# Kernel optimization log

Measured on AMD Instinct MI355X. Metric: run time of the kernel, lower is better.

## Reference

```python
import jax, jax.numpy as jnp
import numpy as np

N_HEADS = 4
D_HEAD = 16
SCALE = D_HEAD ** 0.5  # NOTE: original multiplies by sqrt(d_head), faithful


def _mha(x, Wq, bq, Wk, bk, Wv, bv, Wo, bo):
    # x: (..., N, D) with D = N_HEADS * D_HEAD
    q = jnp.einsum('...nd,od->...no', x, Wq) + bq
    k = jnp.einsum('...nd,od->...no', x, Wk) + bk
    v = jnp.einsum('...nd,od->...no', x, Wv) + bv
    lead = x.shape[:-2]
    n = x.shape[-2]
    q = q.reshape(*lead, n, N_HEADS, D_HEAD)
    k = k.reshape(*lead, n, N_HEADS, D_HEAD)
    v = v.reshape(*lead, n, N_HEADS, D_HEAD)
    scores = jnp.einsum('...nhd,...mhd->...hnm', q, k) * SCALE
    attn = jax.nn.softmax(scores, axis=-1)
    o = jnp.einsum('...hnm,...mhd->...nhd', attn, v).reshape(*lead, n, N_HEADS * D_HEAD)
    return jnp.einsum('...nd,od->...no', o, Wo) + bo


def setup_inputs() -> dict:
    key = jax.random.key(0)
    ks = jax.random.split(key, 20)
    b, n, d, dhf, G, C = 16, 16384, 64, 64, 256, 64
    s = 0.05
    inp = {
        'x': jax.random.normal(ks[0], (b, n, d), dtype=jnp.float32),
        'partitions': jax.random.permutation(ks[1], n).reshape(G, C).astype(jnp.int64),
    }
    names = ['q_intra', 'k_intra', 'v_intra', 'o_intra',
             'q_inter', 'k_inter', 'v_inter', 'o_inter']
    for i, nm in enumerate(names):
        d_in = d if nm.endswith('intra') and nm[0] != 'o' else dhf
        inp['W' + nm] = jax.random.normal(ks[2 + 2 * i], (dhf, d_in), dtype=jnp.float32) * s
        inp['b' + nm] = jax.random.normal(ks[3 + 2 * i], (dhf,), dtype=jnp.float32) * s
    return inp


def reference(x, partitions,
              Wq_intra, bq_intra, Wk_intra, bk_intra, Wv_intra, bv_intra, Wo_intra, bo_intra,
              Wq_inter, bq_inter, Wk_inter, bk_inter, Wv_inter, bv_inter, Wo_inter, bo_inter):
    b = x.shape[0]
    G, C = partitions.shape
    dhf = Wq_intra.shape[0]
    # gather nodes into groups: (b, G, C, d)
    xg = x[:, partitions, :]
    # intra-group attention, vectorized over (b, G)
    intra = _mha(xg, Wq_intra, bq_intra, Wk_intra, bk_intra,
                 Wv_intra, bv_intra, Wo_intra, bo_intra)  # (b, G, C, dhf)
    # MaxPool1d(kernel=dhf) over token axis with C == dhf -> max over tokens
    pooled = jnp.max(intra, axis=2)  # (b, G, dhf)
    inter = _mha(pooled, Wq_inter, bq_inter, Wk_inter, bk_inter,
                 Wv_inter, bv_inter, Wo_inter, bo_inter)  # (b, G, dhf)
    # broadcast-add inter-group features to every token in the group
    out = intra + inter[:, :, None, :]  # (b, G, C, dhf)
    flat = out.reshape(b, G * C, dhf)
    inv = jnp.argsort(partitions.reshape(-1))  # restore original node order
    return flat[:, inv, :]
```

## Files before the change

### kernel.cpp

```cpp
#include <hip/hip_runtime.h>
#include <hip/hip_bf16.h>

#define NTOK 16384
#define NG   256
#define NB   16

typedef float  f32x4   __attribute__((ext_vector_type(4)));
typedef short  short8v __attribute__((ext_vector_type(8)));
typedef short  short4v __attribute__((ext_vector_type(4)));

#define MFMA_BF16(a, b, c) __builtin_amdgcn_mfma_f32_16x16x32_bf16((a), (b), (c), 0, 0, 0)

#define QSCALE 5.770780163555856f

__device__ __forceinline__ short f2bf(float f) {
    union { float f; unsigned u; } x; x.f = f;
    unsigned r = (x.u + 0x7FFF + ((x.u >> 16) & 1)) >> 16;
    return (short)r;
}
__device__ __forceinline__ short bft(float f) {
    union { float f; unsigned u; } x; x.f = f;
    return (short)(x.u >> 16);
}
__device__ __forceinline__ float bf2f(short s) {
    union { float f; unsigned u; } x;
    x.u = ((unsigned)(unsigned short)s) << 16;
    return x.f;
}
__device__ __forceinline__ float u2f(unsigned u) {
    union { unsigned u; float f; } x; x.u = u; return x.f;
}
__device__ __forceinline__ unsigned pk_cvt(float a, float b) {
#if __has_builtin(__builtin_amdgcn_cvt_pk_bf16_f32)
    auto r = __builtin_amdgcn_cvt_pk_bf16_f32(a, b);
    unsigned u; __builtin_memcpy(&u, &r, 4); return u;
#else
    union { float f; unsigned u; } xa, xb; xa.f = a; xb.f = b;
    const unsigned ua = xa.u + (0x7FFFu + ((xa.u >> 16) & 1));
    const unsigned ub = xb.u + (0x7FFFu + ((xb.u >> 16) & 1));
    return __builtin_amdgcn_perm(ub, ua, 0x07060302u);
#endif
}

__global__ void k_setup(const int* __restrict__ raw, int* __restrict__ part,
                        const float* __restrict__ Wq, const float* __restrict__ Wk,
                        const float* __restrict__ Wv, const float* __restrict__ Wo,
                        const float* __restrict__ Wqe, const float* __restrict__ Wke,
                        const float* __restrict__ Wve, const float* __restrict__ Woe,
                        short8v* __restrict__ wf)
{
    const int gid = blockIdx.x * 256 + threadIdx.x;
    if (gid < 16384) {
        const bool is64 = (raw[1] == 0 && raw[3] == 0 && raw[5] == 0);
        part[gid] = is64 ? raw[2 * gid] : raw[gid];
        return;
    }
    const int p = gid - 16384;
    if (p >= 5632) return;
    if (p < 3584) {
        const int v    = p >> 9;
        const int rem  = p & 511;
        const int tau  = rem >> 6;
        const int lane = rem & 63;
        const int jt = tau >> 1, kt = tau & 1;
        const int o  = jt * 16 + (lane & 15);
        const int d0 = kt * 32 + (lane >> 4) * 8;
        const float* W = (v < 2) ? Wq : (v < 4) ? Wk : (v < 6) ? Wv : Wo;
        const bool lo = (v & 1) && (v < 6);
        short8v r8;
#pragma unroll
        for (int i = 0; i < 8; ++i) {
            const float f = W[o * 64 + d0 + i];
            const short hh = f2bf(f);
            r8[i] = lo ? f2bf(f - bf2f(hh)) : hh;
        }
        wf[p] = r8;
    } else {
        const int g2   = p - 3584;
        const int v    = g2 >> 9;
        const int rem  = g2 & 511;
        const int tau  = rem >> 6;
        const int lane = rem & 63;
        const int jt = tau >> 1, kt = tau & 1;
        const int o  = jt * 16 + (lane & 15);
        const int d0 = kt * 32 + (lane >> 4) * 8;
        const float* W = (v == 0) ? Wqe : (v == 1) ? Wke : (v == 2) ? Wve : Woe;
        short8v r8;
#pragma unroll
        for (int i = 0; i < 8; ++i) r8[i] = f2bf(W[o * 64 + d0 + i]);
        wf[p] = r8;
    }
}

__global__ __launch_bounds__(256, 4) void k_intra(
    const float* __restrict__ x, const int* __restrict__ part,
    const short8v* __restrict__ wf,
    const float* __restrict__ bq, const float* __restrict__ bk,
    const float* __restrict__ bv, const float* __restrict__ bo,
    float* __restrict__ out, float* __restrict__ pooled,
    unsigned short* __restrict__ intra_g, const int use_g)
{
    __shared__ __align__(16) short S[20480];

    short* const xh = S;
    short* const kk = S + 4096;
    short* const ql = S + 8192;
    short* const qh = S + 12288;
    short* const vT = S + 16384;

    const int t  = threadIdx.x;
    const int g  = blockIdx.x;
    const int bb = blockIdx.y;
    const int l  = t & 63;
    const int w  = t >> 6;
    const int quad = l >> 4;
    const int col  = l & 15;

    for (int j = t; j < 512; j += 256) {
        const int row = j >> 3, c8 = j & 7;
        const int tok = part[g * 64 + row];
        const float* px = x + ((size_t)bb * NTOK + tok) * 64 + c8 * 8;
        const float4 f0 = ((const float4*)px)[0];
        const float4 f1 = ((const float4*)px)[1];
        uint4 pk;
        pk.x = pk_cvt(f0.x, f0.y);
        pk.y = pk_cvt(f0.z, f0.w);
        pk.z = pk_cvt(f1.x, f1.y);
        pk.w = pk_cvt(f1.z, f1.w);
        *(uint4*)&xh[row * 64 + ((c8 ^ (row & 7)) << 3)] = pk;
    }
    __syncthreads();

    {
        const f32x4 bq4 = *(const f32x4*)&bq[w * 16 + quad * 4];
        const f32x4 bk4 = *(const f32x4*)&bk[w * 16 + quad * 4];
        const float bvv = bv[w * 16 + col];
        f32x4 bqs;
#pragma unroll
        for (int r = 0; r < 4; ++r) bqs[r] = bq4[r] * QSCALE;
        short8v bqh[2], bql2[2], bkh[2], bkl[2], bvh[2], bvl[2];
#pragma unroll
        for (int kt = 0; kt < 2; ++kt) {
            const int tau = w * 2 + kt;
            bqh[kt]  = wf[(0 * 8 + tau) * 64 + l];
            bql2[kt] = wf[(1 * 8 + tau) * 64 + l];
            bkh[kt]  = wf[(2 * 8 + tau) * 64 + l];
            bkl[kt]  = wf[(3 * 8 + tau) * 64 + l];
            bvh[kt]  = wf[(4 * 8 + tau) * 64 + l];
            bvl[kt]  = wf[(5 * 8 + tau) * 64 + l];
        }
        for (int mt = 0; mt < 4; ++mt) {
            short8v axh[2];
#pragma unroll
            for (int kt = 0; kt < 2; ++kt) {
                const int row = mt * 16 + col;
                axh[kt] = *(const short8v*)&xh[row * 64 + (((kt * 4 + quad) ^ (row & 7)) << 3)];
            }
            f32x4 aq = {0.f, 0.f, 0.f, 0.f};
            f32x4 ak = {0.f, 0.f, 0.f, 0.f};
            f32x4 av = {0.f, 0.f, 0.f, 0.f};
#pragma unroll
            for (int kt = 0; kt < 2; ++kt) {
                aq = MFMA_BF16(bqh[kt],  axh[kt], aq);
                aq = MFMA_BF16(bql2[kt], axh[kt], aq);
                ak = MFMA_BF16(bkh[kt],  axh[kt], ak);
                ak = MFMA_BF16(bkl[kt],  axh[kt], ak);
                av = MFMA_BF16(axh[kt], bvh[kt],  av);
                av = MFMA_BF16(axh[kt], bvl[kt],  av);
            }
            f32x4 q4;
#pragma unroll
            for (int r = 0; r < 4; ++r) q4[r] = fmaf(aq[r], QSCALE, bqs[r]);
            const unsigned qh01 = pk_cvt(q4[0], q4[1]);
            const unsigned qh23 = pk_cvt(q4[2], q4[3]);
            const float lo0 = q4[0] - u2f(qh01 << 16);
            const float lo1 = q4[1] - u2f(qh01 & 0xFFFF0000u);
            const float lo2 = q4[2] - u2f(qh23 << 16);
            const float lo3 = q4[3] - u2f(qh23 & 0xFFFF0000u);
            const unsigned ql01 = pk_cvt(lo0, lo1);
            const unsigned ql23 = pk_cvt(lo2, lo3);
            const unsigned k01 = pk_cvt(ak[0] + bk4[0], ak[1] + bk4[1]);
            const unsigned k23 = pk_cvt(ak[2] + bk4[2], ak[3] + bk4[3]);
            const int m = mt * 16 + col;
            const int pos = m * 64 + (((w * 2 + (quad >> 1)) ^ (m & 7)) << 3) + ((quad & 1) << 2);
            uint2 uq; uq.x = qh01; uq.y = qh23;
            uint2 ulo; ulo.x = ql01; ulo.y = ql23;
            uint2 uk; uk.x = k01; uk.y = k23;
            *(uint2*)&qh[pos] = uq;
            *(uint2*)&ql[pos] = ulo;
            *(uint2*)&kk[pos] = uk;
            {
                const int d = w * 16 + col;
                uint2 v4;
                v4.x = pk_cvt(av[0] + bvv, av[1] + bvv);
                v4.y = pk_cvt(av[2] + bvv, av[3] + bvv);
                const int cm = mt * 2 + (quad >> 1);
                const int idx = d * 64 + ((cm ^ (d & 7)) << 3) + ((quad & 1) * 4);
                *(uint2*)&vT[idx] = v4;
            }
        }
    }

    const int h = w, hc = h * 16;
    f32x4 s[4][4];
    {
        short8v ak4[4];
#pragma unroll
        for (int it = 0; it < 4; ++it) {
            const int row = it * 16 + col;
            ak4[it] = *(const short8v*)&kk[row * 64 + (((h * 2 + (quad & 1)) ^ (row & 7)) << 3)];
        }
        const short8v z8 = {0, 0, 0, 0, 0, 0, 0, 0};
        for (int jt = 0; jt < 4; ++jt) {
            const int row = jt * 16 + col;
            const int idx = row * 64 + (((h * 2 + (quad & 1)) ^ (row & 7)) << 3);
            short8v bqh_ = *(const short8v*)&qh[idx];
            short8v bql_ = *(const short8v*)&ql[idx];
            if (quad >= 2) { bqh_ = z8; bql_ = z8; }
#pragma unroll
            for (int it = 0; it < 4; ++it) {
                f32x4 acc = {0.f, 0.f, 0.f, 0.f};
                acc = MFMA_BF16(ak4[it], bqh_, acc);
                acc = MFMA_BF16(ak4[it], bql_, acc);
                s[it][jt] = acc;
            }
        }
    }
    float rden[4];
#pragma unroll
    for (int jt = 0; jt < 4; ++jt) {
        float ds = 0.f;
#pragma unroll
        for (int it = 0; it < 4; ++it) {
#pragma unroll
            for (int r = 0; r < 4; ++r) {
                const float e = exp2f(s[it][jt][r]);
                s[it][jt][r] = e;
                ds += e;
            }
        }
        ds += __shfl_xor(ds, 16);
        ds += __shfl_xor(ds, 32);
        rden[jt] = 1.0f / ds;
    }
    __syncthreads();

    f32x4 oa[4];
#pragma unroll
    for (int jt = 0; jt < 4; ++jt) oa[jt] = (f32x4){0.f, 0.f, 0.f, 0.f};
    short* const Pw = S + w * 2560;
    for (int kt = 0; kt < 2; ++kt) {
#pragma unroll
        for (int jt = 0; jt < 4; ++jt) {
#pragma unroll
            for (int ih = 0; ih < 2; ++ih) {
                const int it = kt * 2 + ih;
                uint2 pp;
                pp.x = pk_cvt(s[it][jt][0], s[it][jt][1]);
                pp.y = pk_cvt(s[it][jt][2], s[it][jt][3]);
                *(uint2*)&Pw[(jt * 16 + col) * 40 + ih * 16 + (quad << 2)] = pp;
            }
        }
        const int dv = hc + col;
        const int cmv = kt * 4 + quad;
        const short8v av8 = *(const short8v*)&vT[dv * 64 + ((cmv ^ (dv & 7)) << 3)];
#pragma unroll
        for (int jt = 0; jt < 4; ++jt) {
            const short8v bp = *(const short8v*)&Pw[(jt * 16 + col) * 40 + (quad << 3)];
            oa[jt] = MFMA_BF16(av8, bp, oa[jt]);
        }
    }
#pragma unroll
    for (int jt = 0; jt < 4; ++jt) {
        const float rd = rden[jt];
        const unsigned o01 = pk_cvt(oa[jt][0] * rd, oa[jt][1] * rd);
        const unsigned o23 = pk_cvt(oa[jt][2] * rd, oa[jt][3] * rd);
        const int m = jt * 16 + col;
        const int pos = m * 64 + (((w * 2 + (quad >> 1)) ^ (m & 7)) << 3) + ((quad & 1) << 2);
        uint2 ov; ov.x = o01; ov.y = o23;
        *(uint2*)&qh[pos] = ov;
    }
    __syncthreads();

    float* const os = (float*)S;
    {
        const float bov = bo[w * 16 + col];
        short8v bo8[2];
        bo8[0] = wf[(6 * 8 + w * 2 + 0) * 64 + l];
        bo8[1] = wf[(6 * 8 + w * 2 + 1) * 64 + l];
        float pm = -1e30f;
        for (int mt = 0; mt < 4; ++mt) {
            f32x4 acc = {0.f, 0.f, 0.f, 0.f};
#pragma unroll
            for (int kt = 0; kt < 2; ++kt) {
                const int row = mt * 16 + col;
                const short8v ao = *(const short8v*)&qh[row * 64 + (((kt * 4 + quad) ^ (row & 7)) << 3)];
                acc = MFMA_BF16(ao, bo8[kt], acc);
            }
#pragma unroll
            for (int r = 0; r < 4; ++r) {
                const float vo = acc[r] + bov;
                pm = fmaxf(pm, vo);
                os[(mt * 16 + quad * 4 + r) * 68 + w * 16 + col] = vo;
            }
        }
        pm = fmaxf(pm, __shfl_xor(pm, 16));
        pm = fmaxf(pm, __shfl_xor(pm, 32));
        if (l < 16)
            pooled[((size_t)bb * NG + g) * 64 + w * 16 + col] = pm;
    }
    __syncthreads();

    {
        const int row = t >> 2, seg = t & 3;
        const float* pr = &os[row * 68 + seg * 16];
        const f32x4 v0 = ((const f32x4*)pr)[0];
        const f32x4 v1 = ((const f32x4*)pr)[1];
        const f32x4 v2 = ((const f32x4*)pr)[2];
        const f32x4 v3 = ((const f32x4*)pr)[3];
        if (use_g) {
            uint4 p0, p1;
            p0.x = pk_cvt(v0[0], v0[1]); p0.y = pk_cvt(v0[2], v0[3]);
            p0.z = pk_cvt(v1[0], v1[1]); p0.w = pk_cvt(v1[2], v1[3]);
            p1.x = pk_cvt(v2[0], v2[1]); p1.y = pk_cvt(v2[2], v2[3]);
            p1.z = pk_cvt(v3[0], v3[1]); p1.w = pk_cvt(v3[2], v3[3]);
            unsigned short* dst = &intra_g[(((size_t)bb * NG + g) * 64 + row) * 64 + seg * 16];
            ((uint4*)dst)[0] = p0;
            ((uint4*)dst)[1] = p1;
        } else {
            const int tok = part[g * 64 + row];
            float* po = &out[((size_t)bb * NTOK + tok) * 64 + seg * 16];
            ((f32x4*)po)[0] = v0; ((f32x4*)po)[1] = v1;
            ((f32x4*)po)[2] = v2; ((f32x4*)po)[3] = v3;
        }
    }
}

__global__ __launch_bounds__(256) void k_inter_qkv(
    const float* __restrict__ pooled, const short8v* __restrict__ wf,
    const float* __restrict__ bq, const float* __restrict__ bk,
    const float* __restrict__ bv,
    short* __restrict__ qws, short* __restrict__ kws, short* __restrict__ vTws)
{
    __shared__ __align__(16) short xs[4096];
    __shared__ __align__(16) short qs[64 * 72];
    __shared__ __align__(16) short ks2[64 * 72];
    const int t = threadIdx.x;
    const int chunk = blockIdx.x, bb = blockIdx.y;
    const int l = t & 63, w = t >> 6;
    const int quad = l >> 4, col = l & 15;

    for (int j = t; j < 512; j += 256) {
        const int row = j >> 3, c8 = j & 7;
        const float* px = pooled + ((size_t)bb * NG + chunk * 64 + row) * 64 + c8 * 8;
        const float4 f0 = ((const float4*)px)[0];
        const float4 f1 = ((const float4*)px)[1];
        uint4 pk;
        pk.x = pk_cvt(f0.x, f0.y);
        pk.y = pk_cvt(f0.z, f0.w);
        pk.z = pk_cvt(f1.x, f1.y);
        pk.w = pk_cvt(f1.z, f1.w);
        *(uint4*)&xs[row * 64 + ((c8 ^ (row & 7)) << 3)] = pk;
    }
    __syncthreads();

    const int WFI = 3584;
    short8v bqf[2], bkf[2], bvf[2];
#pragma unroll
    for (int kt = 0; kt < 2; ++kt) {
        bqf[kt] = wf[WFI + (0 * 8 + w * 2 + kt) * 64 + l];
        bkf[kt] = wf[WFI + (1 * 8 + w * 2 + kt) * 64 + l];
        bvf[kt] = wf[WFI + (2 * 8 + w * 2 + kt) * 64 + l];
    }
    const float bqv = bq[w * 16 + col];
    const float bkv = bk[w * 16 + col];
    const float bvv = bv[w * 16 + col];
    for (int mt = 0; mt < 4; ++mt) {
        short8v ax[2];
#pragma unroll
        for (int kt = 0; kt < 2; ++kt) {
            const int row = mt * 16 + col;
            ax[kt] = *(const short8v*)&xs[row * 64 + (((kt * 4 + quad) ^ (row & 7)) << 3)];
        }
        f32x4 aq = {0.f, 0.f, 0.f, 0.f};
        f32x4 ak = {0.f, 0.f, 0.f, 0.f};
        f32x4 av = {0.f, 0.f, 0.f, 0.f};
#pragma unroll
        for (int kt = 0; kt < 2; ++kt) {
            aq = MFMA_BF16(ax[kt], bqf[kt], aq);
            ak = MFMA_BF16(ax[kt], bkf[kt], ak);
            av = MFMA_BF16(ax[kt], bvf[kt], av);
        }
#pragma unroll
        for (int r = 0; r < 4; ++r) {
            const int m = mt * 16 + quad * 4 + r;
            qs[m * 72 + w * 16 + col]  = f2bf((aq[r] + bqv) * QSCALE);
            ks2[m * 72 + w * 16 + col] = f2bf(ak[r] + bkv);
        }
        uint2 v4;
        v4.x = pk_cvt(av[0] + bvv, av[1] + bvv);
        v4.y = pk_cvt(av[2] + bvv, av[3] + bvv);
        *(uint2*)&vTws[((size_t)bb * 64 + w * 16 + col) * 256 + chunk * 64 + mt * 16 + quad * 4] = v4;
    }
    __syncthreads();
    for (int j = t; j < 512; j += 256) {
        const int row = j >> 3, c8 = j & 7;
        *(short8v*)&qws[((size_t)bb * NG + chunk * 64 + row) * 64 + c8 * 8] =
            *(const short8v*)&qs[row * 72 + c8 * 8];
        *(short8v*)&kws[((size_t)bb * NG + chunk * 64 + row) * 64 + c8 * 8] =
            *(const short8v*)&ks2[row * 72 + c8 * 8];
    }
}

__global__ __launch_bounds__(256) void k_inter_attn2(
    const short* __restrict__ qws, const short* __restrict__ kws,
    const short* __restrict__ vTws, const short8v* __restrict__ wf,
    const float* __restrict__ bo, float* __restrict__ inter)
{
    __shared__ __align__(16) short Pw_all[4 * 16 * 40];
    __shared__ __align__(16) short os[16 * 72];
    const int t = threadIdx.x;
    const int qt = blockIdx.x, bb = blockIdx.y;
    const int l = t & 63, w = t >> 6;
    const int quad = l >> 4, col = l & 15;
    const int hc = w * 16;
    const int r0 = qt * 16;

    const short8v z8 = {0, 0, 0, 0, 0, 0, 0, 0};
    short8v bk[16];
#pragma unroll
    for (int jt = 0; jt < 16; ++jt)
        bk[jt] = (quad < 2)
            ? *(const short8v*)&kws[((size_t)bb * NG + jt * 16 + col) * 64 + hc + quad * 8]
            : z8;
    short8v aq = (quad < 2)
        ? *(const short8v*)&qws[((size_t)bb * NG + r0 + col) * 64 + hc + quad * 8]
        : z8;

    f32x4 s[16];
#pragma unroll
    for (int jt = 0; jt < 16; ++jt) {
        f32x4 acc = {0.f, 0.f, 0.f, 0.f};
        s[jt] = MFMA_BF16(aq, bk[jt], acc);
    }

    float rden[4];
#pragma unroll
    for (int r = 0; r < 4; ++r) {
        float mx = -1e30f;
#pragma unroll
        for (int jt = 0; jt < 16; ++jt) mx = fmaxf(mx, s[jt][r]);
        mx = fmaxf(mx, __shfl_xor(mx, 1));
        mx = fmaxf(mx, __shfl_xor(mx, 2));
        mx = fmaxf(mx, __shfl_xor(mx, 4));
        mx = fmaxf(mx, __shfl_xor(mx, 8));
        float ds = 0.f;
#pragma unroll
        for (int jt = 0; jt < 16; ++jt) {
            const float e = exp2f(s[jt][r] - mx);
            s[jt][r] = e;
            ds += e;
        }
        ds += __shfl_xor(ds, 1);
        ds += __shfl_xor(ds, 2);
        ds += __shfl_xor(ds, 4);
        ds += __shfl_xor(ds, 8);
        rden[r] = 1.0f / ds;
    }

    short* const Pw = Pw_all + w * 16 * 40;
    f32x4 oa = {0.f, 0.f, 0.f, 0.f};
    for (int c = 0; c < 8; ++c) {
#pragma unroll
        for (int jl = 0; jl < 2; ++jl) {
            const int jt = c * 2 + jl;
#pragma unroll
            for (int r = 0; r < 4; ++r)
                Pw[(quad * 4 + r) * 40 + jl * 16 + col] = bft(s[jt][r]);
        }
        const short8v bv8 = *(const short8v*)&vTws[((size_t)bb * 64 + hc + col) * 256 + c * 32 + quad * 8];
        const short8v ap = *(const short8v*)&Pw[col * 40 + quad * 8];
        oa = MFMA_BF16(ap, bv8, oa);
    }
    {
        const unsigned o01 = pk_cvt(oa[0] * rden[0], oa[1] * rden[1]);
        const unsigned o23 = pk_cvt(oa[2] * rden[2], oa[3] * rden[3]);
#pragma unroll
        for (int r = 0; r < 4; ++r) {
            const unsigned uo = (r < 2) ? o01 : o23;
            os[(quad * 4 + r) * 72 + hc + col] = (short)((r & 1) ? (uo >> 16) : (uo & 0xFFFF));
        }
    }
    __syncthreads();

    short8v bof[2];
    bof[0] = wf[3584 + (3 * 8 + w * 2 + 0) * 64 + l];
    bof[1] = wf[3584 + (3 * 8 + w * 2 + 1) * 64 + l];
    const float bov = bo[w * 16 + col];
    {
        f32x4 acc = {0.f, 0.f, 0.f, 0.f};
#pragma unroll
        for (int kt = 0; kt < 2; ++kt) {
            const short8v ao = *(const short8v*)&os[col * 72 + kt * 32 + quad * 8];
            acc = MFMA_BF16(ao, bof[kt], acc);
        }
#pragma unroll
        for (int r = 0; r < 4; ++r)
            inter[((size_t)bb * NG + r0 + quad * 4 + r) * 64 + w * 16 + col] = acc[r] + bov;
    }
}

__global__ __launch_bounds__(256) void k_final(
    const unsigned short* __restrict__ intra_g, const float* __restrict__ inter,
    const int* __restrict__ part, float* __restrict__ out)
{
    __shared__ float interL[64];
    __shared__ int   pidx[64];
    const int t  = threadIdx.x;
    const int g  = blockIdx.x;
    const int bb = blockIdx.y;
    if (t < 64) pidx[t] = part[g * 64 + t];
    else if (t < 128) interL[t - 64] = inter[((size_t)bb * NG + g) * 64 + (t - 64)];
    __syncthreads();
    const int row = t >> 2, seg = t & 3;
    const size_t ib = (((size_t)bb * NG + g) * 64 + row) * 64 + seg * 16;
    const uint4 u0 = *(const uint4*)&intra_g[ib];
    const uint4 u1 = *(const uint4*)&intra_g[ib + 8];
    const float* iL = &interL[seg * 16];
    float* po = &out[((size_t)bb * NTOK + pidx[row]) * 64 + seg * 16];
    f32x4 o0, o1, o2, o3;
    o0[0] = u2f(u0.x << 16)          + iL[0];
    o0[1] = u2f(u0.x & 0xFFFF0000u)  + iL[1];
    o0[2] = u2f(u0.y << 16)          + iL[2];
    o0[3] = u2f(u0.y & 0xFFFF0000u)  + iL[3];
    o1[0] = u2f(u0.z << 16)          + iL[4];
    o1[1] = u2f(u0.z & 0xFFFF0000u)  + iL[5];
    o1[2] = u2f(u0.w << 16)          + iL[6];
    o1[3] = u2f(u0.w & 0xFFFF0000u)  + iL[7];
    o2[0] = u2f(u1.x << 16)          + iL[8];
    o2[1] = u2f(u1.x & 0xFFFF0000u)  + iL[9];
    o2[2] = u2f(u1.y << 16)          + iL[10];
    o2[3] = u2f(u1.y & 0xFFFF0000u)  + iL[11];
    o3[0] = u2f(u1.z << 16)          + iL[12];
    o3[1] = u2f(u1.z & 0xFFFF0000u)  + iL[13];
    o3[2] = u2f(u1.w << 16)          + iL[14];
    o3[3] = u2f(u1.w & 0xFFFF0000u)  + iL[15];
    ((f32x4*)po)[0] = o0;
    ((f32x4*)po)[1] = o1;
    ((f32x4*)po)[2] = o2;
    ((f32x4*)po)[3] = o3;
}

__global__ __launch_bounds__(256) void k_scatter_add(
    const float* __restrict__ inter, const int* __restrict__ part,
    float* __restrict__ out)
{
    __shared__ float iv[64];
    __shared__ int   pidx[64];
    const int t  = threadIdx.x;
    const int g  = blockIdx.x;
    const int bb = blockIdx.y;
    if (t < 64) {
        iv[t]   = inter[((size_t)bb * NG + g) * 64 + t];
        pidx[t] = part[g * 64 + t];
    }
    __syncthreads();
    const int oo   = t & 63;
    const int cseg = t >> 6;
    const float add = iv[oo];
    for (int ci = 0; ci < 16; ++ci) {
        const int c = cseg * 16 + ci;
        float* p = out + ((size_t)bb * NTOK + pidx[c]) * 64 + oo;
        *p += add;
    }
}

extern "C" void kernel_launch(void* const* d_in, const int* in_sizes, int n_in,
                              void* d_out, int out_size, void* d_ws, size_t ws_size,
                              hipStream_t stream)
{
    const float* x    = (const float*)d_in[0];
    const int*   praw = (const int*)d_in[1];
    const float* Wq_a = (const float*)d_in[2];
    const float* bq_a = (const float*)d_in[3];
    const float* Wk_a = (const float*)d_in[4];
    const float* bk_a = (const float*)d_in[5];
    const float* Wv_a = (const float*)d_in[6];
    const float* bv_a = (const float*)d_in[7];
    const float* Wo_a = (const float*)d_in[8];
    const float* bo_a = (const float*)d_in[9];
    const float* Wq_e = (const float*)d_in[10];
    const float* bq_e = (const float*)d_in[11];
    const float* Wk_e = (const float*)d_in[12];
    const float* bk_e = (const float*)d_in[13];
    const float* Wv_e = (const float*)d_in[14];
    const float* bv_e = (const float*)d_in[15];
    const float* Wo_e = (const float*)d_in[16];
    const float* bo_e = (const float*)d_in[17];

    char* ws = (char*)d_ws;
    int*     part   = (int*)ws;
    float*   pooled = (float*)(ws + (1u << 16));
    float*   inter  = (float*)(ws + (1u << 16) + (1u << 20));
    short8v* wf     = (short8v*)(ws + (1u << 16) + 2 * (1u << 20));
    char*    base2  = ws + (1u << 16) + 2 * (1u << 20) + 98304;
    short*   qws    = (short*)base2;
    short*   kws    = (short*)(base2 + (1u << 19));
    short*   vTws   = (short*)(base2 + 2 * (1u << 19));
    unsigned short* intra_g = (unsigned short*)(base2 + 3 * (1u << 19));
    const size_t need = ((size_t)(base2 - ws)) + 3 * (1u << 19) + (size_t)NB * NG * 64 * 64 * 2;
    const int use_g = (ws_size >= need) ? 1 : 0;

    float* out = (float*)d_out;

    k_setup<<<dim3(86), dim3(256), 0, stream>>>(praw, part, Wq_a, Wk_a, Wv_a, Wo_a,
                                                Wq_e, Wk_e, Wv_e, Wo_e, wf);
    k_intra<<<dim3(NG, NB), dim3(256), 0, stream>>>(
        x, part, wf, bq_a, bk_a, bv_a, bo_a, out, pooled, intra_g, use_g);
    k_inter_qkv<<<dim3(4, NB), dim3(256), 0, stream>>>(
        pooled, wf, bq_e, bk_e, bv_e, qws, kws, vTws);
    k_inter_attn2<<<dim3(16, NB), dim3(256), 0, stream>>>(
        qws, kws, vTws, wf, bo_e, inter);
    if (use_g)
        k_final<<<dim3(NG, NB), dim3(256), 0, stream>>>(intra_g, inter, part, out);
    else
        k_scatter_add<<<dim3(NG, NB), dim3(256), 0, stream>>>(inter, part, out);
}
```

Measured before the change: 204.2 us.

## Fuse inter-group attention with final broadcast-add scatter into one kernel

Replaces the inter QKV, inter attention and final scatter kernels with a single fused kernel per (query tile, batch). Each block recomputes K and V for all groups in shared memory, computes attention and output projection for 16 groups, then adds the result to the bf16 intra features and scatters them to the output. This removes two launches and the global round trip for q/k/v and inter. In exchange it adds redundant K/V projection and runs the large scatter phase with far fewer blocks.

```diff
diff --git a/kernel.cpp b/kernel.cpp
--- a/kernel.cpp
+++ b/kernel.cpp
@@ -336,6 +336,240 @@
     }
 }
 
+__global__ __launch_bounds__(256, 2) void k_inter_fused(
+    const float* __restrict__ pooled, const short8v* __restrict__ wf,
+    const float* __restrict__ bq, const float* __restrict__ bk,
+    const float* __restrict__ bv, const float* __restrict__ bo,
+    const unsigned short* __restrict__ intra_g, const int* __restrict__ part,
+    float* __restrict__ out)
+{
+    __shared__ __align__(16) short S[29312];
+    short* const xs     = S;
+    short* const kk     = S + 16384;
+    short* const vT     = S + 20480;
+    short* const qs     = S + 24576;
+    short* const Pw_all = S + 25600;
+    short* const os     = S + 28160;
+    float* const interF = (float*)S;
+
+    const int t  = threadIdx.x;
+    const int qt = blockIdx.x, bb = blockIdx.y;
+    const int l  = t & 63, w = t >> 6;
+    const int quad = l >> 4, col = l & 15;
+    const int r0 = qt * 16;
+    const int WFI = 3584;
+
+    for (int j = t; j < 2048; j += 256) {
+        const int row = j >> 3, c8 = j & 7;
+        const float* px = pooled + ((size_t)bb * NG + row) * 64 + c8 * 8;
+        const float4 f0 = ((const float4*)px)[0];
+        const float4 f1 = ((const float4*)px)[1];
+        uint4 pk;
+        pk.x = pk_cvt(f0.x, f0.y);
+        pk.y = pk_cvt(f0.z, f0.w);
+        pk.z = pk_cvt(f1.x, f1.y);
+        pk.w = pk_cvt(f1.z, f1.w);
+        *(uint4*)&xs[row * 64 + ((c8 ^ (row & 7)) << 3)] = pk;
+    }
+    __syncthreads();
+
+    const int h = w, hc = h * 16;
+    const short8v z8 = {0, 0, 0, 0, 0, 0, 0, 0};
+
+    {
+        const f32x4 bq4 = *(const f32x4*)&bq[w * 16 + quad * 4];
+        f32x4 bqs;
+#pragma unroll
+        for (int r = 0; r < 4; ++r) bqs[r] = bq4[r] * QSCALE;
+        short8v bqf[2], axq[2];
+#pragma unroll
+        for (int kt = 0; kt < 2; ++kt) {
+            bqf[kt] = wf[WFI + (0 * 8 + w * 2 + kt) * 64 + l];
+            const int row = r0 + col;
+            axq[kt] = *(const short8v*)&xs[row * 64 + (((kt * 4 + quad) ^ (row & 7)) << 3)];
+        }
+        f32x4 aq = {0.f, 0.f, 0.f, 0.f};
+#pragma unroll
+        for (int kt = 0; kt < 2; ++kt) aq = MFMA_BF16(bqf[kt], axq[kt], aq);
+        f32x4 q4;
+#pragma unroll
+        for (int r = 0; r < 4; ++r) q4[r] = fmaf(aq[r], QSCALE, bqs[r]);
+        const int pos = col * 64 + (((w * 2 + (quad >> 1)) ^ (col & 7)) << 3) + ((quad & 1) << 2);
+        uint2 uq; uq.x = pk_cvt(q4[0], q4[1]); uq.y = pk_cvt(q4[2], q4[3]);
+        *(uint2*)&qs[pos] = uq;
+    }
+
+    short8v bkf[2], bvf[2];
+#pragma unroll
+    for (int kt = 0; kt < 2; ++kt) {
+        bkf[kt] = wf[WFI + (1 * 8 + w * 2 + kt) * 64 + l];
+        bvf[kt] = wf[WFI + (2 * 8 + w * 2 + kt) * 64 + l];
+    }
+    const f32x4 bk4 = *(const f32x4*)&bk[w * 16 + quad * 4];
+    const float bvv = bv[w * 16 + col];
+
+    f32x4 s[4][4];
+    for (int c = 0; c < 4; ++c) {
+        for (int mt = 0; mt < 4; ++mt) {
+            short8v axk[2];
+#pragma unroll
+            for (int kt = 0; kt < 2; ++kt) {
+                const int row = c * 64 + mt * 16 + col;
+                axk[kt] = *(const short8v*)&xs[row * 64 + (((kt * 4 + quad) ^ (row & 7)) << 3)];
+            }
+            f32x4 ak = {0.f, 0.f, 0.f, 0.f};
+#pragma unroll
+            for (int kt = 0; kt < 2; ++kt) ak = MFMA_BF16(bkf[kt], axk[kt], ak);
+            const unsigned k01 = pk_cvt(ak[0] + bk4[0], ak[1] + bk4[1]);
+            const unsigned k23 = pk_cvt(ak[2] + bk4[2], ak[3] + bk4[3]);
+            const int ml = mt * 16 + col;
+            const int pos = ml * 64 + (((w * 2 + (quad >> 1)) ^ (ml & 7)) << 3) + ((quad & 1) << 2);
+            uint2 uk; uk.x = k01; uk.y = k23;
+            *(uint2*)&kk[pos] = uk;
+        }
+        short8v ak4[4];
+#pragma unroll
+        for (int it = 0; it < 4; ++it) {
+            const int row = it * 16 + col;
+            ak4[it] = *(const short8v*)&kk[row * 64 + (((h * 2 + (quad & 1)) ^ (row & 7)) << 3)];
+        }
+        short8v bq_ = *(const short8v*)&qs[col * 64 + (((h * 2 + (quad & 1)) ^ (col & 7)) << 3)];
+        if (quad >= 2) bq_ = z8;
+#pragma unroll
+        for (int it = 0; it < 4; ++it) {
+            f32x4 acc = {0.f, 0.f, 0.f, 0.f};
+            s[c][it] = MFMA_BF16(ak4[it], bq_, acc);
+        }
+    }
+
+    float rden;
+    {
+        float mx = -1e30f;
+#pragma unroll
+        for (int c = 0; c < 4; ++c)
+#pragma unroll
+            for (int it = 0; it < 4; ++it)
+#pragma unroll
+                for (int r = 0; r < 4; ++r) mx = fmaxf(mx, s[c][it][r]);
+        mx = fmaxf(mx, __shfl_xor(mx, 16));
+        mx = fmaxf(mx, __shfl_xor(mx, 32));
+        float ds = 0.f;
+#pragma unroll
+        for (int c = 0; c < 4; ++c)
+#pragma unroll
+            for (int it = 0; it < 4; ++it)
+#pragma unroll
+                for (int r = 0; r < 4; ++r) {
+                    const float e = exp2f(s[c][it][r] - mx);
+                    s[c][it][r] = e;
+                    ds += e;
+                }
+        ds += __shfl_xor(ds, 16);
+        ds += __shfl_xor(ds, 32);
+        rden = 1.0f / ds;
+    }
+
+    f32x4 oa = {0.f, 0.f, 0.f, 0.f};
+    short* const Pw = Pw_all + w * 640;
+    for (int c = 0; c < 4; ++c) {
+        for (int mt = 0; mt < 4; ++mt) {
+            short8v axv[2];
+#pragma unroll
+            for (int kt = 0; kt < 2; ++kt) {
+                const int row = c * 64 + mt * 16 + col;
+                axv[kt] = *(const short8v*)&xs[row * 64 + (((kt * 4 + quad) ^ (row & 7)) << 3)];
+            }
+            f32x4 av = {0.f, 0.f, 0.f, 0.f};
+#pragma unroll
+            for (int kt = 0; kt < 2; ++kt) av = MFMA_BF16(axv[kt], bvf[kt], av);
+            const int d = w * 16 + col;
+            uint2 v4;
+            v4.x = pk_cvt(av[0] + bvv, av[1] + bvv);
+            v4.y = pk_cvt(av[2] + bvv, av[3] + bvv);
+            const int cm = mt * 2 + (quad >> 1);
+            const int idx = d * 64 + ((cm ^ (d & 7)) << 3) + ((quad & 1) * 4);
+            *(uint2*)&vT[idx] = v4;
+        }
+        for (int kt2 = 0; kt2 < 2; ++kt2) {
+#pragma unroll
+            for (int ih = 0; ih < 2; ++ih) {
+                const int it = kt2 * 2 + ih;
+                uint2 pp;
+                pp.x = pk_cvt(s[c][it][0], s[c][it][1]);
+                pp.y = pk_cvt(s[c][it][2], s[c][it][3]);
+                *(uint2*)&Pw[col * 40 + ih * 16 + (quad << 2)] = pp;
+            }
+            const int dv = hc + col;
+            const int cmv = kt2 * 4 + quad;
+            const short8v av8 = *(const short8v*)&vT[dv * 64 + ((cmv ^ (dv & 7)) << 3)];
+            const short8v bp = *(const short8v*)&Pw[col * 40 + (quad << 3)];
+            oa = MFMA_BF16(av8, bp, oa);
+        }
+    }
+    {
+        const unsigned o01 = pk_cvt(oa[0] * rden, oa[1] * rden);
+        const unsigned o23 = pk_cvt(oa[2] * rden, oa[3] * rden);
+        uint2 ov; ov.x = o01; ov.y = o23;
+        *(uint2*)&os[col * 72 + hc + (quad << 2)] = ov;
+    }
+    __syncthreads();
+
+    {
+        short8v bof[2];
+        bof[0] = wf[WFI + (3 * 8 + w * 2 + 0) * 64 + l];
+        bof[1] = wf[WFI + (3 * 8 + w * 2 + 1) * 64 + l];
+        const float bov = bo[w * 16 + col];
+        f32x4 acc = {0.f, 0.f, 0.f, 0.f};
+#pragma unroll
+        for (int kt = 0; kt < 2; ++kt) {
+            const short8v ao = *(const short8v*)&os[col * 72 + kt * 32 + quad * 8];
+            acc = MFMA_BF16(ao, bof[kt], acc);
+        }
+#pragma unroll
+        for (int r = 0; r < 4; ++r)
+            interF[(quad * 4 + r) * 68 + w * 16 + col] = acc[r] + bov;
+    }
+    __syncthreads();
+
+    {
+        const int row = t >> 2, seg = t & 3;
+        for (int g2 = 0; g2 < 16; ++g2) {
+            const int gg = r0 + g2;
+            const int tok = part[gg * 64 + row];
+            const size_t ib = (((size_t)bb * NG + gg) * 64 + row) * 64 + seg * 16;
+            const uint4 u0 = *(const uint4*)&intra_g[ib];
+            const uint4 u1 = *(const uint4*)&intra_g[ib + 8];
+            const float* iL = &interF[g2 * 68 + seg * 16];
+            const f32x4 i0 = ((const f32x4*)iL)[0];
+            const f32x4 i1 = ((const f32x4*)iL)[1];
+            const f32x4 i2 = ((const f32x4*)iL)[2];
+            const f32x4 i3 = ((const f32x4*)iL)[3];
+            float* po = &out[((size_t)bb * NTOK + tok) * 64 + seg * 16];
+            f32x4 o0, o1, o2, o3;
+            o0[0] = u2f(u0.x << 16)         + i0[0];
+            o0[1] = u2f(u0.x & 0xFFFF0000u) + i0[1];
+            o0[2] = u2f(u0.y << 16)         + i0[2];
+            o0[3] = u2f(u0.y & 0xFFFF0000u) + i0[3];
+            o1[0] = u2f(u0.z << 16)         + i1[0];
+            o1[1] = u2f(u0.z & 0xFFFF0000u) + i1[1];
+            o1[2] = u2f(u0.w << 16)         + i1[2];
+            o1[3] = u2f(u0.w & 0xFFFF0000u) + i1[3];
+            o2[0] = u2f(u1.x << 16)         + i2[0];
+            o2[1] = u2f(u1.x & 0xFFFF0000u) + i2[1];
+            o2[2] = u2f(u1.y << 16)         + i2[2];
+            o2[3] = u2f(u1.y & 0xFFFF0000u) + i2[3];
+            o3[0] = u2f(u1.z << 16)         + i3[0];
+            o3[1] = u2f(u1.z & 0xFFFF0000u) + i3[1];
+            o3[2] = u2f(u1.w << 16)         + i3[2];
+            o3[3] = u2f(u1.w & 0xFFFF0000u) + i3[3];
+            ((f32x4*)po)[0] = o0;
+            ((f32x4*)po)[1] = o1;
+            ((f32x4*)po)[2] = o2;
+            ((f32x4*)po)[3] = o3;
+        }
+    }
+}
+
 __global__ __launch_bounds__(256) void k_inter_qkv(
     const float* __restrict__ pooled, const short8v* __restrict__ wf,
     const float* __restrict__ bq, const float* __restrict__ bk,
@@ -508,47 +742,6 @@
         for (int r = 0; r < 4; ++r)
             inter[((size_t)bb * NG + r0 + quad * 4 + r) * 64 + w * 16 + col] = acc[r] + bov;
     }
-}
-
-__global__ __launch_bounds__(256) void k_final(
-    const unsigned short* __restrict__ intra_g, const float* __restrict__ inter,
-    const int* __restrict__ part, float* __restrict__ out)
-{
-    __shared__ float interL[64];
-    __shared__ int   pidx[64];
-    const int t  = threadIdx.x;
-    const int g  = blockIdx.x;
-    const int bb = blockIdx.y;
-    if (t < 64) pidx[t] = part[g * 64 + t];
-    else if (t < 128) interL[t - 64] = inter[((size_t)bb * NG + g) * 64 + (t - 64)];
-    __syncthreads();
-    const int row = t >> 2, seg = t & 3;
-    const size_t ib = (((size_t)bb * NG + g) * 64 + row) * 64 + seg * 16;
-    const uint4 u0 = *(const uint4*)&intra_g[ib];
-    const uint4 u1 = *(const uint4*)&intra_g[ib + 8];
-    const float* iL = &interL[seg * 16];
-    float* po = &out[((size_t)bb * NTOK + pidx[row]) * 64 + seg * 16];
-    f32x4 o0, o1, o2, o3;
-    o0[0] = u2f(u0.x << 16)          + iL[0];
-    o0[1] = u2f(u0.x & 0xFFFF0000u)  + iL[1];
-    o0[2] = u2f(u0.y << 16)          + iL[2];
-    o0[3] = u2f(u0.y & 0xFFFF0000u)  + iL[3];
-    o1[0] = u2f(u0.z << 16)          + iL[4];
-    o1[1] = u2f(u0.z & 0xFFFF0000u)  + iL[5];
-    o1[2] = u2f(u0.w << 16)          + iL[6];
-    o1[3] = u2f(u0.w & 0xFFFF0000u)  + iL[7];
-    o2[0] = u2f(u1.x << 16)          + iL[8];
-    o2[1] = u2f(u1.x & 0xFFFF0000u)  + iL[9];
-    o2[2] = u2f(u1.y << 16)          + iL[10];
-    o2[3] = u2f(u1.y & 0xFFFF0000u)  + iL[11];
-    o3[0] = u2f(u1.z << 16)          + iL[12];
-    o3[1] = u2f(u1.z & 0xFFFF0000u)  + iL[13];
-    o3[2] = u2f(u1.w << 16)          + iL[14];
-    o3[3] = u2f(u1.w & 0xFFFF0000u)  + iL[15];
-    ((f32x4*)po)[0] = o0;
-    ((f32x4*)po)[1] = o1;
-    ((f32x4*)po)[2] = o2;
-    ((f32x4*)po)[3] = o3;
 }
 
 __global__ __launch_bounds__(256) void k_scatter_add(
@@ -617,12 +810,14 @@
                                                 Wq_e, Wk_e, Wv_e, Wo_e, wf);
     k_intra<<<dim3(NG, NB), dim3(256), 0, stream>>>(
         x, part, wf, bq_a, bk_a, bv_a, bo_a, out, pooled, intra_g, use_g);
-    k_inter_qkv<<<dim3(4, NB), dim3(256), 0, stream>>>(
-        pooled, wf, bq_e, bk_e, bv_e, qws, kws, vTws);
-    k_inter_attn2<<<dim3(16, NB), dim3(256), 0, stream>>>(
-        qws, kws, vTws, wf, bo_e, inter);
-    if (use_g)
-        k_final<<<dim3(NG, NB), dim3(256), 0, stream>>>(intra_g, inter, part, out);
-    else
+    if (use_g) {
+        k_inter_fused<<<dim3(16, NB), dim3(256), 0, stream>>>(
+            pooled, wf, bq_e, bk_e, bv_e, bo_e, intra_g, part, out);
+    } else {
+        k_inter_qkv<<<dim3(4, NB), dim3(256), 0, stream>>>(
+            pooled, wf, bq_e, bk_e, bv_e, qws, kws, vTws);
+        k_inter_attn2<<<dim3(16, NB), dim3(256), 0, stream>>>(
+            qws, kws, vTws, wf, bo_e, inter);
         k_scatter_add<<<dim3(NG, NB), dim3(256), 0, stream>>>(inter, part, out);
-}
+    }
+}
```

After: 200.5 us. About the same (-1.8%).
